# Kernel optimization log

Measured on AMD Instinct MI355X. Metric: run time of the kernel, lower is better.

The kernel has to match this reference:

```python
import jax, jax.numpy as jnp
import numpy as np

T, E, H = 65536, 512, 512  # seq_len, embedding_size, hidden_size (kernel_size=2)


def setup_inputs() -> dict:
    key = jax.random.key(0)
    k1, k2 = jax.random.split(key)
    x = jax.random.normal(k1, (T, E), dtype=jnp.float32)
    # nn.Linear(2*E, 3*H): weight [3H, 2E], bias [3H]. Store transposed for x @ W.
    W = jax.random.normal(k2, (2 * E, 3 * H), dtype=jnp.float32) * 0.02
    b = jnp.zeros((3 * H,), dtype=jnp.float32)
    return {"input": x, "W": W, "b": b}


def reference(input, W, b):
    x = input
    t, e = x.shape
    h_dim = W.shape[1] // 3
    # Shift input by one step (zero-padded) and concat: conv over kernel_size=2 window.
    x_prev = jnp.concatenate([jnp.zeros((1, e), x.dtype), x[:-1]], axis=0)  # [T, E]
    gates = jnp.concatenate([x, x_prev], axis=1) @ W + b  # [T, 3H]
    z = jnp.tanh(gates[:, :h_dim])                # cell candidate
    f = jax.nn.sigmoid(gates[:, h_dim:2 * h_dim])  # forget gate
    o = jax.nn.sigmoid(gates[:, 2 * h_dim:])       # output gate

    # fo-pool recurrence: c_t = f_t * c_{t-1} + (1 - f_t) * z_t ; h_t = o_t * c_t
    def step(c, zfo):
        z_t, f_t, o_t = zfo
        c_new = f_t * c + (1.0 - f_t) * z_t
        return c_new, (c_new, o_t * c_new)

    c0 = jnp.zeros((h_dim,), x.dtype)
    _, (cells, hiddens) = jax.lax.scan(step, c0, (z, f, o))
    # Match torch: (hidden_temp [T,H], h [1,H], c [1,H])
    return hiddens, hiddens[-1:], cells[-1:]
```

## Files before the change

kernel.cpp:

```cpp
#include <hip/hip_runtime.h>


#define T_LEN 65536
#define H3    1536
#define LC    64
#define NCHUNK 1024

typedef float f32x4 __attribute__((ext_vector_type(4)));
typedef short bf16x8 __attribute__((ext_vector_type(8)));

__device__ __forceinline__ unsigned short f2bf(float f) {
    unsigned int x = __builtin_bit_cast(unsigned int, f);
    x += 0x7fffu + ((x >> 16) & 1u);
    return (unsigned short)(x >> 16);
}
__device__ __forceinline__ float bf2f(unsigned short u) {
    return __builtin_bit_cast(float, ((unsigned int)u) << 16);
}
__device__ __forceinline__ float fsig(float x) {
    return __builtin_amdgcn_rcpf(1.f + __builtin_amdgcn_exp2f(-1.44269504f * x));
}
__device__ __forceinline__ float ftanh(float x) {
    return 2.f * __builtin_amdgcn_rcpf(1.f + __builtin_amdgcn_exp2f(-2.88539008f * x)) - 1.f;
}

__device__ __forceinline__ void gload_lds16(const void* g, void* l) {
    __builtin_amdgcn_global_load_lds((const __attribute__((address_space(1))) void*)g,
                                     (__attribute__((address_space(3))) void*)l, 16, 0, 0);
}

#define VM2()   asm volatile("s_waitcnt vmcnt(2)" ::: "memory")
#define VM0()   asm volatile("s_waitcnt vmcnt(0)" ::: "memory")
#define BARX()  __builtin_amdgcn_s_barrier()

__global__ void prep_x(const float* __restrict__ x, unsigned short* __restrict__ xp) {
    const long long nq = (512LL + (long long)T_LEN * 512) / 4;
    for (long long q = (long long)blockIdx.x * blockDim.x + threadIdx.x; q < nq;
         q += (long long)gridDim.x * blockDim.x) {
        ushort4 u;
        if (q < 128) {
            u.x = 0; u.y = 0; u.z = 0; u.w = 0;
        } else {
            const float4 v = *reinterpret_cast<const float4*>(x + q * 4 - 512);
            u.x = f2bf(v.x); u.y = f2bf(v.y); u.z = f2bf(v.z); u.w = f2bf(v.w);
        }
        *reinterpret_cast<ushort4*>(xp + q * 4) = u;
    }
}

__global__ void prep_w(const float* __restrict__ W, unsigned short* __restrict__ Wt) {
    const int n_el = 1024 * H3;
    for (int i = blockIdx.x * blockDim.x + threadIdx.x; i < n_el;
         i += gridDim.x * blockDim.x) {
        const int k = i / H3, n = i - k * H3;
        Wt[n * 1024 + k] = f2bf(W[i]);
    }
}

__global__ __launch_bounds__(256, 2) void gemm_gates(
    const unsigned short* __restrict__ xp,
    const unsigned short* __restrict__ Wt,
    const float* __restrict__ bias,
    unsigned short* __restrict__ zfo)
{
    __shared__ unsigned short Alds[4][128 * 32];
    __shared__ unsigned short Blds[2][256 * 32];

    const int tid  = threadIdx.x;
    const int lane = tid & 63;
    const int w    = tid >> 6;
    const int wm   = w >> 1, wn = w & 1;

    const int flat = blockIdx.y * gridDim.x + blockIdx.x;
    const int idx  = (flat & 7) * 384 + (flat >> 3);
    const int nb   = (idx % 6) * 256;
    const long long t0 = (long long)(idx / 6) * 128;

    const int srow_l = lane >> 2;
    const int scol   = (((lane & 3) ^ ((lane >> 3) & 3)) * 8);

    const unsigned short* gA = xp + (t0 + w * 16 + srow_l) * 512 + 512 + scol;
    const unsigned short* gB = Wt + (long long)(nb + w * 16 + srow_l) * 1024 + scol;

    auto stageA = [&](unsigned short* Al) {
        gload_lds16(gA,              Al + (w * 16) * 32);
        gload_lds16(gA + 64 * 512,   Al + (64 + w * 16) * 32);
    };
    auto stageB = [&](unsigned short* Bl) {
        gload_lds16(gB,              Bl + (w * 16) * 32);
        gload_lds16(gB + 64 * 1024,  Bl + (64 + w * 16) * 32);
        gload_lds16(gB + 128 * 1024, Bl + (128 + w * 16) * 32);
        gload_lds16(gB + 192 * 1024, Bl + (192 + w * 16) * 32);
    };

    const int arow  = lane & 15;
    const int swzco = (((lane >> 4) ^ ((arow >> 1) & 3)) * 8);

    f32x4 acc[4][8] = {};

    auto compute = [&](const unsigned short* Al, const unsigned short* Bl) {
        bf16x8 af[4], bfr[8];
        #pragma unroll
        for (int m = 0; m < 4; ++m)
            af[m] = *reinterpret_cast<const bf16x8*>(Al + (wm * 64 + m * 16 + arow) * 32 + swzco);
        #pragma unroll
        for (int n = 0; n < 8; ++n)
            bfr[n] = *reinterpret_cast<const bf16x8*>(Bl + (wn * 128 + n * 16 + arow) * 32 + swzco);
        #pragma unroll
        for (int n = 0; n < 8; ++n)
            #pragma unroll
            for (int m = 0; m < 4; ++m)
                acc[m][n] = __builtin_amdgcn_mfma_f32_16x16x32_bf16(af[m], bfr[n], acc[m][n], 0, 0, 0);
    };

    stageB(Blds[0]); gB += 32;
    stageA(Alds[0]); gA += 32;
    stageA(Alds[1]); gA += 32;
    stageA(Alds[2]); gA += 32;
    asm volatile("s_waitcnt vmcnt(4)" ::: "memory");
    BARX();

    for (int base = 0; base < 28; base += 4) {
        #pragma unroll
        for (int k = 0; k < 4; ++k) {
            stageB(Blds[(k + 1) & 1]); gB += 32;
            stageA(Alds[(k + 3) & 3]);
            gA += (base + k == 12) ? -992 : 32;
            compute(Alds[k & 3], Blds[k & 1]);
            VM2();
            BARX();
        }
    }
    {
        stageB(Blds[1]); gB += 32;
        stageA(Alds[3]);
        compute(Alds[0], Blds[0]);
        VM2(); BARX();
    }
    {
        stageB(Blds[0]); gB += 32;
        compute(Alds[1], Blds[1]);
        VM0(); BARX();
    }
    {
        stageB(Blds[1]);
        compute(Alds[2], Blds[0]);
        VM0(); BARX();
    }
    compute(Alds[3], Blds[1]);

    const int cls = nb >> 9;
    #pragma unroll
    for (int n = 0; n < 8; ++n) {
        const int col = nb + wn * 128 + n * 16 + arow;
        const float bn_ = bias[col];
        #pragma unroll
        for (int m = 0; m < 4; ++m) {
            const long long row0 = t0 + wm * 64 + m * 16 + (lane >> 4) * 4;
            #pragma unroll
            for (int j = 0; j < 4; ++j) {
                float v = acc[m][n][j] + bn_;
                v = (cls == 0) ? ftanh(v) : fsig(v);
                zfo[(row0 + j) * H3 + col] = f2bf(v);
            }
        }
    }
}

__global__ void scan_pass1(const unsigned short* __restrict__ zfo,
                           float* __restrict__ P, float* __restrict__ L) {
    const int chunk = blockIdx.x;
    const int c4    = threadIdx.x;
    const unsigned short* base = zfo + (long long)chunk * LC * H3 + c4 * 4;
    float c[4] = {0.f, 0.f, 0.f, 0.f};
    float p[4] = {1.f, 1.f, 1.f, 1.f};
    for (int t = 0; t < LC; ++t) {
        const unsigned short* row = base + t * H3;
        const ushort4 uz = *reinterpret_cast<const ushort4*>(row);
        const ushort4 uf = *reinterpret_cast<const ushort4*>(row + 512);
        const float z[4] = {bf2f(uz.x), bf2f(uz.y), bf2f(uz.z), bf2f(uz.w)};
        const float f[4] = {bf2f(uf.x), bf2f(uf.y), bf2f(uf.z), bf2f(uf.w)};
        #pragma unroll
        for (int j = 0; j < 4; ++j) {
            c[j] = fmaf(f[j], c[j] - z[j], z[j]);
            p[j] *= f[j];
        }
    }
    #pragma unroll
    for (int j = 0; j < 4; ++j) {
        P[chunk * 512 + c4 * 4 + j] = p[j];
        L[chunk * 512 + c4 * 4 + j] = c[j];
    }
}

__global__ __launch_bounds__(1024) void scan_pass2(
    const float* __restrict__ P, const float* __restrict__ L,
    float* __restrict__ carry, float* __restrict__ out) {
    const int ch = blockIdx.x;
    const int k  = threadIdx.x;
    __shared__ float sP[1024], sL[1024];
    float p = P[k * 512 + ch];
    float l = L[k * 512 + ch];
    sP[k] = p; sL[k] = l;
    __syncthreads();
    for (int d = 1; d < 1024; d <<= 1) {
        float pp = 1.f, ll = 0.f;
        if (k >= d) { pp = sP[k - d]; ll = sL[k - d]; }
        __syncthreads();
        l = fmaf(p, ll, l);
        p = p * pp;
        sP[k] = p; sL[k] = l;
        __syncthreads();
    }
    carry[k * 512 + ch] = (k == 0) ? 0.f : sL[k - 1];
    if (k == 1023) out[(long long)T_LEN * 512 + 512 + ch] = l;
}

__global__ void scan_pass3(const unsigned short* __restrict__ zfo,
                           const float* __restrict__ carry,
                           float* __restrict__ out) {
    const int chunk = blockIdx.x;
    const int c4    = threadIdx.x;
    const unsigned short* base = zfo + (long long)chunk * LC * H3 + c4 * 4;
    float c[4], h[4] = {0.f, 0.f, 0.f, 0.f};
    #pragma unroll
    for (int j = 0; j < 4; ++j) c[j] = carry[chunk * 512 + c4 * 4 + j];
    float4* outp = reinterpret_cast<float4*>(out + (long long)chunk * LC * 512) + c4;
    for (int t = 0; t < LC; ++t) {
        const unsigned short* row = base + t * H3;
        const ushort4 uz = *reinterpret_cast<const ushort4*>(row);
        const ushort4 uf = *reinterpret_cast<const ushort4*>(row + 512);
        const ushort4 uo = *reinterpret_cast<const ushort4*>(row + 1024);
        const float z[4] = {bf2f(uz.x), bf2f(uz.y), bf2f(uz.z), bf2f(uz.w)};
        const float f[4] = {bf2f(uf.x), bf2f(uf.y), bf2f(uf.z), bf2f(uf.w)};
        const float o[4] = {bf2f(uo.x), bf2f(uo.y), bf2f(uo.z), bf2f(uo.w)};
        #pragma unroll
        for (int j = 0; j < 4; ++j) {
            c[j] = fmaf(f[j], c[j] - z[j], z[j]);
            h[j] = o[j] * c[j];
        }
        float4 hv; hv.x = h[0]; hv.y = h[1]; hv.z = h[2]; hv.w = h[3];
        outp[t * 128] = hv;
    }
    if (chunk == NCHUNK - 1) {
        #pragma unroll
        for (int j = 0; j < 4; ++j)
            out[(long long)T_LEN * 512 + c4 * 4 + j] = h[j];
    }
}

extern "C" void kernel_launch(void* const* d_in, const int* in_sizes, int n_in,
                              void* d_out, int out_size, void* d_ws, size_t ws_size,
                              hipStream_t stream) {
    const float* x = (const float*)d_in[0];
    const float* W = (const float*)d_in[1];
    const float* b = (const float*)d_in[2];
    float* out = (float*)d_out;

    char* ws = (char*)d_ws;
    unsigned short* xp  = (unsigned short*)(ws);
    unsigned short* Wt  = (unsigned short*)(ws + 67110912LL);
    unsigned short* zfo = (unsigned short*)(ws + 70256640LL);
    float* P     = (float*)(ws);
    float* L     = (float*)(ws + 4194304LL);
    float* carry = (float*)(ws + 8388608LL);

    prep_x<<<4096, 256, 0, stream>>>(x, xp);
    prep_w<<<768, 256, 0, stream>>>(W, Wt);

    dim3 gg(H3 / 256, T_LEN / 128, 1);
    gemm_gates<<<gg, 256, 0, stream>>>(xp, Wt, b, zfo);

    scan_pass1<<<NCHUNK, 128, 0, stream>>>(zfo, P, L);
    scan_pass2<<<512, 1024, 0, stream>>>(P, L, carry, out);
    scan_pass3<<<NCHUNK, 128, 0, stream>>>(zfo, carry, out);
}
```

Before: 377.8 us.

## Fuse x fp32-to-bf16 conversion into GEMM A-tile loading, drop prep_x kernel

After: 433.8 us. +14.8%, slower.

```diff
diff --git a/kernel.cpp b/kernel.cpp
--- a/kernel.cpp
+++ b/kernel.cpp
@@ -1,4 +1,5 @@
 #include <hip/hip_runtime.h>
+#include <hip/hip_bf16.h>
 
 
 #define T_LEN 65536
@@ -29,24 +30,24 @@
                                      (__attribute__((address_space(3))) void*)l, 16, 0, 0);
 }
 
-#define VM2()   asm volatile("s_waitcnt vmcnt(2)" ::: "memory")
+__device__ __forceinline__ bf16x8 pack8(float4 a, float4 b) {
+    union { bf16x8 v; unsigned short u[8]; } r;
+    r.u[0] = __builtin_bit_cast(unsigned short, __float2bfloat16(a.x));
+    r.u[1] = __builtin_bit_cast(unsigned short, __float2bfloat16(a.y));
+    r.u[2] = __builtin_bit_cast(unsigned short, __float2bfloat16(a.z));
+    r.u[3] = __builtin_bit_cast(unsigned short, __float2bfloat16(a.w));
+    r.u[4] = __builtin_bit_cast(unsigned short, __float2bfloat16(b.x));
+    r.u[5] = __builtin_bit_cast(unsigned short, __float2bfloat16(b.y));
+    r.u[6] = __builtin_bit_cast(unsigned short, __float2bfloat16(b.z));
+    r.u[7] = __builtin_bit_cast(unsigned short, __float2bfloat16(b.w));
+    return r.v;
+}
+
+#define VM4()   asm volatile("s_waitcnt vmcnt(4)" ::: "memory")
 #define VM0()   asm volatile("s_waitcnt vmcnt(0)" ::: "memory")
+#define LGKM0() asm volatile("s_waitcnt lgkmcnt(0)" ::: "memory")
 #define BARX()  __builtin_amdgcn_s_barrier()
-
-__global__ void prep_x(const float* __restrict__ x, unsigned short* __restrict__ xp) {
-    const long long nq = (512LL + (long long)T_LEN * 512) / 4;
-    for (long long q = (long long)blockIdx.x * blockDim.x + threadIdx.x; q < nq;
-         q += (long long)gridDim.x * blockDim.x) {
-        ushort4 u;
-        if (q < 128) {
-            u.x = 0; u.y = 0; u.z = 0; u.w = 0;
-        } else {
-            const float4 v = *reinterpret_cast<const float4*>(x + q * 4 - 512);
-            u.x = f2bf(v.x); u.y = f2bf(v.y); u.z = f2bf(v.z); u.w = f2bf(v.w);
-        }
-        *reinterpret_cast<ushort4*>(xp + q * 4) = u;
-    }
-}
+#define ORD()   asm volatile("" ::: "memory")
 
 __global__ void prep_w(const float* __restrict__ W, unsigned short* __restrict__ Wt) {
     const int n_el = 1024 * H3;
@@ -58,12 +59,12 @@
 }
 
 __global__ __launch_bounds__(256, 2) void gemm_gates(
-    const unsigned short* __restrict__ xp,
+    const float* __restrict__ x,
     const unsigned short* __restrict__ Wt,
     const float* __restrict__ bias,
     unsigned short* __restrict__ zfo)
 {
-    __shared__ unsigned short Alds[4][128 * 32];
+    __shared__ unsigned short Alds[2][128 * 32];
     __shared__ unsigned short Blds[2][256 * 32];
 
     const int tid  = threadIdx.x;
@@ -77,14 +78,29 @@
     const long long t0 = (long long)(idx / 6) * 128;
 
     const int srow_l = lane >> 2;
+    const int aRow   = w * 16 + srow_l;
+    const bool azero = (t0 == 0) && (aRow == 0);
     const int scol   = (((lane & 3) ^ ((lane >> 3) & 3)) * 8);
 
-    const unsigned short* gA = xp + (t0 + w * 16 + srow_l) * 512 + 512 + scol;
-    const unsigned short* gB = Wt + (long long)(nb + w * 16 + srow_l) * 1024 + scol;
-
-    auto stageA = [&](unsigned short* Al) {
-        gload_lds16(gA,              Al + (w * 16) * 32);
-        gload_lds16(gA + 64 * 512,   Al + (64 + w * 16) * 32);
+    const float* gA = x + (t0 + aRow) * 512 + (lane & 3) * 8;
+    const unsigned short* gB = Wt + (long long)(nb + aRow) * 1024 + scol;
+
+    auto issueA = [&](float4* r, int s) {
+        if (azero && s >= 16) {
+            r[0] = float4{0.f, 0.f, 0.f, 0.f};
+            r[1] = float4{0.f, 0.f, 0.f, 0.f};
+        } else {
+            r[0] = *reinterpret_cast<const float4*>(gA);
+            r[1] = *reinterpret_cast<const float4*>(gA + 4);
+        }
+        r[2] = *reinterpret_cast<const float4*>(gA + 64 * 512);
+        r[3] = *reinterpret_cast<const float4*>(gA + 64 * 512 + 4);
+    };
+    auto writeA = [&](unsigned short* Al, const float4* r) {
+        const int sw = (lane & 3) ^ ((srow_l >> 1) & 3);
+        unsigned short* a0 = Al + aRow * 32 + sw * 8;
+        *reinterpret_cast<bf16x8*>(a0)           = pack8(r[0], r[1]);
+        *reinterpret_cast<bf16x8*>(a0 + 64 * 32) = pack8(r[2], r[3]);
     };
     auto stageB = [&](unsigned short* Bl) {
         gload_lds16(gB,              Bl + (w * 16) * 32);
@@ -113,41 +129,44 @@
                 acc[m][n] = __builtin_amdgcn_mfma_f32_16x16x32_bf16(af[m], bfr[n], acc[m][n], 0, 0, 0);
     };
 
+    float4 rP[4], rQ[4];
+
+    issueA(rP, 0); gA += 32;
+    ORD();
     stageB(Blds[0]); gB += 32;
-    stageA(Alds[0]); gA += 32;
-    stageA(Alds[1]); gA += 32;
-    stageA(Alds[2]); gA += 32;
-    asm volatile("s_waitcnt vmcnt(4)" ::: "memory");
-    BARX();
-
-    for (int base = 0; base < 28; base += 4) {
-        #pragma unroll
-        for (int k = 0; k < 4; ++k) {
-            stageB(Blds[(k + 1) & 1]); gB += 32;
-            stageA(Alds[(k + 3) & 3]);
-            gA += (base + k == 12) ? -992 : 32;
-            compute(Alds[k & 3], Blds[k & 1]);
-            VM2();
-            BARX();
-        }
-    }
-    {
-        stageB(Blds[1]); gB += 32;
-        stageA(Alds[3]);
-        compute(Alds[0], Blds[0]);
-        VM2(); BARX();
-    }
-    {
-        stageB(Blds[0]); gB += 32;
-        compute(Alds[1], Blds[1]);
-        VM0(); BARX();
-    }
-    {
-        stageB(Blds[1]);
-        compute(Alds[2], Blds[0]);
-        VM0(); BARX();
-    }
-    compute(Alds[3], Blds[1]);
+    ORD();
+    issueA(rQ, 1); gA += 32;
+    VM4();
+    writeA(Alds[0], rP);
+    LGKM0(); BARX();
+
+    for (int tp = 0; tp < 30; tp += 2) {
+        {
+            stageB(Blds[1]); gB += 32;
+            ORD();
+            issueA(rP, tp + 2); gA += 32;
+            compute(Alds[0], Blds[0]);
+            VM4();
+            writeA(Alds[1], rQ);
+            LGKM0(); BARX();
+        }
+        {
+            stageB(Blds[0]); gB += 32;
+            ORD();
+            issueA(rQ, tp + 3);
+            gA += (tp == 12) ? -992 : 32;
+            compute(Alds[1], Blds[1]);
+            VM4();
+            writeA(Alds[0], rP);
+            LGKM0(); BARX();
+        }
+    }
+    stageB(Blds[1]);
+    compute(Alds[0], Blds[0]);
+    VM0();
+    writeA(Alds[1], rQ);
+    LGKM0(); BARX();
+    compute(Alds[1], Blds[1]);
 
     const int cls = nb >> 9;
     #pragma unroll
@@ -258,18 +277,16 @@
     float* out = (float*)d_out;
 
     char* ws = (char*)d_ws;
-    unsigned short* xp  = (unsigned short*)(ws);
     unsigned short* Wt  = (unsigned short*)(ws + 67110912LL);
     unsigned short* zfo = (unsigned short*)(ws + 70256640LL);
     float* P     = (float*)(ws);
     float* L     = (float*)(ws + 4194304LL);
     float* carry = (float*)(ws + 8388608LL);
 
-    prep_x<<<4096, 256, 0, stream>>>(x, xp);
     prep_w<<<768, 256, 0, stream>>>(W, Wt);
 
     dim3 gg(H3 / 256, T_LEN / 128, 1);
-    gemm_gates<<<gg, 256, 0, stream>>>(xp, Wt, b, zfo);
+    gemm_gates<<<gg, 256, 0, stream>>>(x, Wt, b, zfo);
 
     scan_pass1<<<NCHUNK, 128, 0, stream>>>(zfo, P, L);
     scan_pass2<<<512, 1024, 0, stream>>>(P, L, carry, out);
```
